# Optimization experiments

Measured on AMD Instinct MI355X. Metric: run time of the kernel, lower is better.

Reference implementation:

```python
import jax, jax.numpy as jnp
import numpy as np

N = 768          # nodes
E_HALF = 12288   # undirected edges (both directions added -> E = 24576)
P = 4096         # query pairs
H = 32           # hidden_dim_1wl == hidden_dim_2wl
MAX_X = 100
EPS = 1e-5
LAYER1 = 2


def setup_inputs() -> dict:
    key = jax.random.key(0)
    ks = jax.random.split(key, 12)
    s = 0.1
    x = jax.random.randint(ks[0], (N,), 0, MAX_X + 1)
    half = jax.random.randint(ks[1], (2, E_HALF), 0, N)
    ei = jnp.concatenate([half, half[::-1]], axis=1)          # symmetric edge set [2,E]
    pos = jax.random.randint(ks[2], (P, 2), 0, N)
    emb = jax.random.normal(ks[3], (MAX_X + 1, H)) * s
    gcn_W = jax.random.normal(ks[4], (LAYER1, H, H)) * s
    gcn_b = jnp.zeros((LAYER1, H))
    mlp1_W = jax.random.normal(ks[5], (2 * H, H)) * s
    mlp1_b = jnp.zeros((H,))
    mlp2_W = jax.random.normal(ks[6], (2 * H, H)) * s
    mlp2_b = jnp.zeros((H,))
    mlp3_W = jax.random.normal(ks[7], (H + 1, H)) * s
    mlp3_b = jnp.zeros((H,))
    lin_W = jax.random.normal(ks[8], (2 * H, 1)) * s
    lin_b = jnp.zeros((1,))
    return dict(x=x, ei=ei, pos=pos, emb=emb, gcn_W=gcn_W, gcn_b=gcn_b,
                mlp1_W=mlp1_W, mlp1_b=mlp1_b, mlp2_W=mlp2_W, mlp2_b=mlp2_b,
                mlp3_W=mlp3_W, mlp3_b=mlp3_b, lin_W=lin_W, lin_b=lin_b)


def _graph_norm(h):
    # PyG-style GraphNorm with default params (mean_scale=1, weight=1, bias=0)
    h = h - h.mean(0)
    return h * jax.lax.rsqrt((h * h).mean(0) + EPS)


def reference(x, ei, pos, emb, gcn_W, gcn_b, mlp1_W, mlp1_b,
              mlp2_W, mlp2_b, mlp3_W, mlp3_b, lin_W, lin_b):
    n = x.shape[0]
    d = emb.shape[1]
    h = emb[x]                                                 # [n,H] (dropout=0)
    # --- GCNConv stack: Ahat = D^-1/2 (A+I) D^-1/2 ---
    A = jnp.zeros((n, n), h.dtype).at[ei[0], ei[1]].set(1.0)
    Ahat = A + jnp.eye(n, dtype=h.dtype)
    dinv = jax.lax.rsqrt(Ahat.sum(1))
    An = Ahat * dinv[:, None] * dinv[None, :]
    for l in range(gcn_W.shape[0]):
        h = An @ (h @ gcn_W[l]) + gcn_b[l]
        h = jax.nn.relu(_graph_norm(h))                        # GraphNorm + ReLU
    # --- pair features ---
    xx = h[pos[:, 0]] * h[pos[:, 1]]                           # [P,H]
    val = jnp.concatenate([h[ei[0]], h[ei[1]]], 1)             # [E,2H]
    xe = jax.nn.relu(val @ mlp1_W + mlp1_b)                    # mlps_1
    mul = jax.nn.relu(val @ mlp2_W + mlp2_b)                   # mlps_2[0]
    # --- sparse_bmm as dense [n,n,d] contraction (coalesce sums duplicates -> .add) ---
    Xd = jnp.zeros((n, n, d), h.dtype).at[ei[0], ei[1]].add(xe)
    Md = jnp.zeros((n, n, d), h.dtype).at[ei[0], ei[1]].add(mul)
    C = jnp.einsum('ikd,kjd->ijd', Xd, Md)                     # x_{ij} = sum_k x_{ik}*mul_{kj}
    # support of the sparse result: 2-hop pairs union original edges (sparse_cat)
    adj_b = jnp.zeros((n, n), bool).at[ei[0], ei[1]].set(True)
    af = adj_b.astype(h.dtype)
    mask = ((af @ af) > 0) | adj_b
    ind = af[..., None]                                        # ones-column for original edges
    value = jnp.concatenate([C, ind], -1)                      # [n,n,H+1]
    z = value @ mlp3_W + mlp3_b                                # mlps_3[0]
    # GraphNorm over the edge support only (faithful to sparse values())
    m = mask.astype(h.dtype)[..., None]
    cnt = m.sum()
    mean = (z * m).sum((0, 1)) / cnt
    z = z - mean
    var = ((z * z) * m).sum((0, 1)) / cnt
    z = jax.nn.relu(z * jax.lax.rsqrt(var + EPS))
    # x * sm: multiply by transposed values; zero outside support (= add_zero)
    sym = z * jnp.swapaxes(z, 0, 1) * m
    pair = sym[pos[:, 0], pos[:, 1]]                           # [P,H] (edge_list gather)
    out = jnp.concatenate([pair, xx], 1) @ lin_W + lin_b       # lin_dir -> [P,1]
    return out
```

## Files before the change

### kernel.cpp

```cpp
#include <hip/hip_runtime.h>
#include <hip/hip_bf16.h>

#define NN 768
#define NE 24576
#define NPOS 4096
#define NCELL (NN*NN)
#define NBLK 2304
#define NBIG 2304
#define BCELLS 256
#define CAP 8
#define NREP 16

typedef __hip_bfloat16 bf16;

__device__ __forceinline__ float ldf(const void* p, int i, int mode) {
    return mode ? __bfloat162float(((const bf16*)p)[i]) : ((const float*)p)[i];
}
__device__ __forceinline__ float aread(float* p) { return atomicAdd(p, 0.f); }
__device__ __forceinline__ int areadi(int* p) { return atomicAdd(p, 0); }

template<int D, int HALF>
__device__ __forceinline__ void redRound(float* v, int lane) {
#pragma unroll
    for (int i = 0; i < HALF; i++) {
        float snd = (lane & D) ? v[i] : v[i + HALF];
        float r = __shfl_xor(snd, D);
        v[i] = ((lane & D) ? v[i + HALF] : v[i]) + r;
    }
}

#define DOT4(Z, A, W) Z += A.x * W.x + A.y * W.y + A.z * W.z + A.w * W.w

#define GATH(rec, q0,q1,q2,q3,q4,q5,q6,q7) { \
    const float4* xr = xep4 + (int)((unsigned)(rec).x & 0x7FFFu) * 8; \
    const float4* mr = mulp4 + (int)((unsigned)(rec).y & 0x7FFFu) * 8; \
    float4 xv0 = xr[0], xv1 = xr[1], xv2 = xr[2], xv3 = xr[3]; \
    float4 xv4 = xr[4], xv5 = xr[5], xv6 = xr[6], xv7 = xr[7]; \
    float4 mv0 = mr[0], mv1 = mr[1], mv2 = mr[2], mv3 = mr[3]; \
    float4 mv4 = mr[4], mv5 = mr[5], mv6 = mr[6], mv7 = mr[7]; \
    q0.x += xv0.x*mv0.x; q0.y += xv0.y*mv0.y; q0.z += xv0.z*mv0.z; q0.w += xv0.w*mv0.w; \
    q1.x += xv1.x*mv1.x; q1.y += xv1.y*mv1.y; q1.z += xv1.z*mv1.z; q1.w += xv1.w*mv1.w; \
    q2.x += xv2.x*mv2.x; q2.y += xv2.y*mv2.y; q2.z += xv2.z*mv2.z; q2.w += xv2.w*mv2.w; \
    q3.x += xv3.x*mv3.x; q3.y += xv3.y*mv3.y; q3.z += xv3.z*mv3.z; q3.w += xv3.w*mv3.w; \
    q4.x += xv4.x*mv4.x; q4.y += xv4.y*mv4.y; q4.z += xv4.z*mv4.z; q4.w += xv4.w*mv4.w; \
    q5.x += xv5.x*mv5.x; q5.y += xv5.y*mv5.y; q5.z += xv5.z*mv5.z; q5.w += xv5.w*mv5.w; \
    q6.x += xv6.x*mv6.x; q6.y += xv6.y*mv6.y; q6.z += xv6.z*mv6.z; q6.w += xv6.w*mv6.w; \
    q7.x += xv7.x*mv7.x; q7.y += xv7.y*mv7.y; q7.z += xv7.z*mv7.z; q7.w += xv7.w*mv7.w; }

__global__ void k_scatter(const int* __restrict__ ei, int* __restrict__ cell, int* __restrict__ rowlen,
                          int* __restrict__ row_ptr, float* __restrict__ dinv, int* __restrict__ dc,
                          const void* __restrict__ gW, const void* __restrict__ gB,
                          const void* __restrict__ m1W, const void* __restrict__ m1B,
                          const void* __restrict__ m2W, const void* __restrict__ m2B,
                          const void* __restrict__ m3W, const void* __restrict__ m3B,
                          const void* __restrict__ lW,  const void* __restrict__ lB,
                          const void* __restrict__ emb, int* __restrict__ modeg,
                          float* __restrict__ gwf, float* __restrict__ gbf,
                          float* __restrict__ w1f, float* __restrict__ b1f,
                          float* __restrict__ w2f, float* __restrict__ b2f,
                          float* __restrict__ w3q, float* __restrict__ linf, float* __restrict__ linb) {
    int t = threadIdx.x;
    if (blockIdx.x == 96) {
        __shared__ int bad;
        if (t == 0) bad = 0;
        __syncthreads();
        int local = 0;
        for (int i = t; i < 3232; i += 256) {
            float a = fabsf(__bfloat162float(((const bf16*)emb)[i]));
            if (!(a < 100.f)) local = 1;
        }
        if (local) atomicOr(&bad, 1);
        __syncthreads();
        int mode = bad ? 0 : 1;
        if (t == 0) *modeg = mode;
        for (int i = t; i < 2048; i += 256) {
            gwf[i] = ldf(gW, i, mode);
            w1f[i] = ldf(m1W, i, mode);
            w2f[i] = ldf(m2W, i, mode);
        }
        for (int i = t; i < 64; i += 256) { gbf[i] = ldf(gB, i, mode); linf[i] = ldf(lW, i, mode); }
        if (t < 32) { b1f[t] = ldf(m1B, t, mode); b2f[t] = ldf(m2B, t, mode); }
        for (int i = t; i < 1056; i += 256) { int c = i >> 5, d = i & 31; w3q[d * 36 + c] = ldf(m3W, i, mode); }
        if (t < 32) { w3q[t * 36 + 33] = ldf(m3B, t, mode); w3q[t * 36 + 34] = 0.f; w3q[t * 36 + 35] = 0.f; }
        if (t == 0) linb[0] = ldf(lB, 0, mode);
        return;
    }
    __shared__ int amlast;
    __shared__ int sI[256];
    int e = blockIdx.x * 256 + t;
    int a = ei[e], b = ei[NE + e];
    if ((unsigned)a < (unsigned)NN && (unsigned)b < (unsigned)NN) {
        int old = atomicAdd(&cell[a * NN + b], 1);
        if (old == 0) atomicAdd(&rowlen[a], 1);
    }
    __syncthreads();
    if (t == 0) { __threadfence(); amlast = (atomicAdd(dc, 1) == 95) ? 1 : 0; }
    __syncthreads();
    if (!amlast) return;
    int i0 = 3 * t;
    int r0 = areadi(&rowlen[i0]), r1 = areadi(&rowlen[i0 + 1]), r2 = areadi(&rowlen[i0 + 2]);
    dinv[i0]     = rsqrtf((float)r0 + 1.f);
    dinv[i0 + 1] = rsqrtf((float)r1 + 1.f);
    dinv[i0 + 2] = rsqrtf((float)r2 + 1.f);
    int s3 = r0 + r1 + r2;
    sI[t] = s3;
    __syncthreads();
    for (int off = 1; off < 256; off <<= 1) {
        int tmp = (t >= off) ? sI[t - off] : 0;
        __syncthreads();
        sI[t] += tmp;
        __syncthreads();
    }
    int excl = sI[t] - s3;
    row_ptr[i0] = excl;
    row_ptr[i0 + 1] = excl + r0;
    row_ptr[i0 + 2] = excl + r0 + r1;
    if (t == 255) row_ptr[NN] = sI[255];
}

__global__ void k_fill(int* __restrict__ cell, const int* __restrict__ row_ptr, int* __restrict__ cursor,
                       int* __restrict__ col_idx, float* __restrict__ cntv, int* __restrict__ pr_row,
                       const int* __restrict__ rowlen, int* __restrict__ rtot,
                       const int* __restrict__ x, const void* __restrict__ emb,
                       const int* __restrict__ modep, float* __restrict__ bufA) {
    int t = threadIdx.x;
    int b = blockIdx.x;
    if (b < NBLK) {
        int idx = b * 256 + t;
        int i = idx / NN;
        int j = idx - i * NN;
        int cv = cell[idx];
        if (cv > 0) {
            int p = row_ptr[i] + atomicAdd(&cursor[i], 1);
            col_idx[p] = j; cntv[p] = (float)cv; pr_row[p] = i;
            cell[idx] = p;
            atomicAdd(&rtot[i], rowlen[j]);
        } else cell[idx] = -1;
    } else {
        int idx = (b - NBLK) * 256 + t;
        int i = idx >> 5, k = idx & 31;
        int xi = x[i]; if (xi < 0) xi = 0; if (xi > 100) xi = 100;
        bufA[idx] = ldf(emb, xi * 32 + k, *modep);
    }
}

__global__ void k_aggmw0(const int* __restrict__ rtot, int* __restrict__ row_base,
                         const int* __restrict__ row_ptr, const int* __restrict__ col_idx,
                         const float* __restrict__ bufA, const float* __restrict__ dinv,
                         const float* __restrict__ gwf, const float* __restrict__ gbf,
                         float* __restrict__ bufB) {
    int t = threadIdx.x;
    if (blockIdx.x == 0) {
        __shared__ int sI[256];
        int r3[3]; int s3 = 0;
#pragma unroll
        for (int q = 0; q < 3; q++) { r3[q] = rtot[3 * t + q]; s3 += r3[q]; }
        sI[t] = s3;
        __syncthreads();
        for (int off = 1; off < 256; off <<= 1) {
            int tmp = (t >= off) ? sI[t - off] : 0;
            __syncthreads();
            sI[t] += tmp;
            __syncthreads();
        }
        int run = sI[t] - s3;
        row_base[3 * t] = run;
        row_base[3 * t + 1] = run + r3[0];
        row_base[3 * t + 2] = run + r3[0] + r3[1];
        return;
    }
    __shared__ float sg[8][32];
    int li = t >> 5, k = t & 31;
    int i = (blockIdx.x - 1) * 8 + li;
    int base = row_ptr[i], len = row_ptr[i + 1] - base;
    float di = dinv[i];
    float acc = di * bufA[i * 32 + k];
    for (int e = 0; e < len; e++) {
        int c = col_idx[base + e];
        acc += dinv[c] * bufA[c * 32 + k];
    }
    sg[li][k] = di * acc;
    __syncthreads();
    int d = k;
    float s = gbf[d];
#pragma unroll
    for (int kk = 0; kk < 32; kk++) s += sg[li][kk] * gwf[kk * 32 + d];
    bufB[i * 32 + d] = s;
}

__global__ void k_hist(const int* __restrict__ row_ptr, const int* __restrict__ col_idx,
                       const int* __restrict__ row_base,
                       int* __restrict__ pcur, int2* __restrict__ paths2, int cap,
                       const float* __restrict__ bufB, float* __restrict__ nrm0) {
    int t = threadIdx.x;
    if (blockIdx.x == NN) {
        __shared__ float r1[256], r2[256];
        int dd = t & 31, g = t >> 5;
        float s = 0.f, s2 = 0.f;
        for (int r = g; r < NN; r += 8) { float v = bufB[r * 32 + dd]; s += v; s2 += v * v; }
        r1[t] = s; r2[t] = s2;
        __syncthreads();
        if (t < 32) {
            float a = 0.f, b2 = 0.f;
            for (int k = 0; k < 8; k++) { a += r1[k * 32 + t]; b2 += r2[k * 32 + t]; }
            float mean = a / (float)NN;
            float var = b2 / (float)NN - mean * mean;
            nrm0[t] = mean;
            nrm0[32 + t] = rsqrtf(fmaxf(var, 0.f) + 1e-5f);
        }
        return;
    }
    __shared__ int hist[NN];
    __shared__ int sc[256];
    int i = blockIdx.x;
    int base = row_ptr[i], len = row_ptr[i + 1] - base;
    int rb = row_base[i];
    int wave = t >> 6, lane = t & 63;
    for (int j = t; j < NN; j += 256) hist[j] = 0;
    __syncthreads();
    for (int ee = wave; ee < len; ee += 4) {
        int k = col_idx[base + ee];
        int kb = row_ptr[k], ke = row_ptr[k + 1];
        for (int e = kb + lane; e < ke; e += 64) atomicAdd(&hist[col_idx[e]], 1);
    }
    __syncthreads();
    int h0 = hist[3 * t], h1 = hist[3 * t + 1], h2 = hist[3 * t + 2];
    int s3 = h0 + h1 + h2;
    sc[t] = s3;
    __syncthreads();
    for (int off = 1; off < 256; off <<= 1) {
        int tmp = (t >= off) ? sc[t - off] : 0;
        __syncthreads();
        sc[t] += tmp;
        __syncthreads();
    }
    int excl = sc[t] - s3;
    int n0 = i * NN + 3 * t;
    pcur[n0]     = rb + excl + h0;
    pcur[n0 + 1] = rb + excl + h0 + h1;
    pcur[n0 + 2] = rb + excl + h0 + h1 + h2;
    hist[3 * t] = excl;
    hist[3 * t + 1] = excl + h0;
    hist[3 * t + 2] = excl + h0 + h1;
    __syncthreads();
    for (int ee = wave; ee < len; ee += 4) {
        int e1 = base + ee;
        int k = col_idx[e1];
        int kb = row_ptr[k], ke = row_ptr[k + 1];
        for (int e = kb + lane; e < ke; e += 64) {
            int j = col_idx[e];
            int slot = rb + atomicAdd(&hist[j], 1);
            if (slot < cap) {
                unsigned n2 = (unsigned)(i * NN + j);
                paths2[slot] = make_int2((int)((unsigned)e1 | ((n2 & 0x1FFFFu) << 15)),
                                         (int)((unsigned)e  | ((n2 >> 17) << 15)));
            }
        }
    }
}

__global__ void k_aggmw1(const int* __restrict__ row_ptr, const int* __restrict__ col_idx,
                         const float* __restrict__ bufB, const float* __restrict__ nrm0,
                         const float* __restrict__ dinv,
                         const float* __restrict__ gwf, const float* __restrict__ gbf,
                         float* __restrict__ bufA, float* __restrict__ stats1) {
    __shared__ float sg[8][32];
    int t = threadIdx.x;
    int li = t >> 5, k = t & 31;
    int i = blockIdx.x * 8 + li;
    float mk = nrm0[k], rk = nrm0[32 + k];
    int base = row_ptr[i], len = row_ptr[i + 1] - base;
    float di = dinv[i];
    float acc = di * fmaxf((bufB[i * 32 + k] - mk) * rk, 0.f);
    for (int e = 0; e < len; e++) {
        int c = col_idx[base + e];
        acc += dinv[c] * fmaxf((bufB[c * 32 + k] - mk) * rk, 0.f);
    }
    sg[li][k] = di * acc;
    __syncthreads();
    int d = k;
    const float* W = gwf + 1024;
    float s = gbf[32 + d];
#pragma unroll
    for (int kk = 0; kk < 32; kk++) s += sg[li][kk] * W[kk * 32 + d];
    bufA[i * 32 + d] = s;
    __syncthreads();
    sg[li][d] = s;
    __syncthreads();
    if (t < 32) {
        float ps = 0.f, ps2 = 0.f;
#pragma unroll
        for (int q = 0; q < 8; q++) { float v = sg[q][t]; ps += v; ps2 += v * v; }
        float* rep = stats1 + (blockIdx.x & (NREP - 1)) * 80;
        atomicAdd(&rep[t], ps);
        atomicAdd(&rep[32 + t], ps2);
    }
}

__global__ void k_emlp(const float* __restrict__ bufA, const float* __restrict__ stats1,
                       const int* __restrict__ row_ptr, const int* __restrict__ col_idx,
                       const int* __restrict__ pr_row, const float* __restrict__ cntv,
                       const float* __restrict__ w1f, const float* __restrict__ b1f,
                       const float* __restrict__ w2f, const float* __restrict__ b2f,
                       float* __restrict__ xep, float* __restrict__ mulp, float* __restrict__ h) {
    __shared__ float nmean[32], nrstd[32];
    int t = threadIdx.x;
    int b = blockIdx.x;
    if (t < 32) {
        float s = 0.f, s2 = 0.f;
#pragma unroll
        for (int r = 0; r < NREP; r++) { s += stats1[r * 80 + t]; s2 += stats1[r * 80 + 32 + t]; }
        float mean = s / (float)NN;
        float var = s2 / (float)NN - mean * mean;
        nmean[t] = mean;
        nrstd[t] = rsqrtf(fmaxf(var, 0.f) + 1e-5f);
    }
    __syncthreads();
    if (b < 3072) {
        int d = t & 31;
        int p = b * 8 + (t >> 5);
        if (p >= row_ptr[NN]) {
            if (p < NE) { xep[p * 32 + d] = 0.f; mulp[p * 32 + d] = 0.f; }
            return;
        }
        int i = pr_row[p], j = col_idx[p];
        float a1 = b1f[d], a2 = b2f[d];
#pragma unroll
        for (int c = 0; c < 32; c++) {
            float hv = fmaxf((bufA[i * 32 + c] - nmean[c]) * nrstd[c], 0.f);
            a1 += hv * w1f[c * 32 + d];
            a2 += hv * w2f[c * 32 + d];
        }
#pragma unroll
        for (int c = 0; c < 32; c++) {
            float hv = fmaxf((bufA[j * 32 + c] - nmean[c]) * nrstd[c], 0.f);
            a1 += hv * w1f[(32 + c) * 32 + d];
            a2 += hv * w2f[(32 + c) * 32 + d];
        }
        float cv = cntv[p];
        xep[p * 32 + d]  = cv * fmaxf(a1, 0.f);
        mulp[p * 32 + d] = cv * fmaxf(a2, 0.f);
    } else {
        int idx = (b - 3072) * 256 + t;
        int d = idx & 31;
        h[idx] = fmaxf((bufA[idx] - nmean[d]) * nrstd[d], 0.f);
    }
}

__global__ __launch_bounds__(256, 4) void k_big(const int* __restrict__ pcur,
                                                const int2* __restrict__ paths2,
                                                const int* __restrict__ cellA,
                                                const float* __restrict__ xep, const float* __restrict__ mulp,
                                                const float* __restrict__ w3q,
                                                float* __restrict__ stats, int* __restrict__ done,
                                                float* __restrict__ nrm, int cap) {
    __shared__ float Cb[BCELLS * 36];
    __shared__ float sS1[32], sS2[32];
    __shared__ float sCm;
    __shared__ int amlast;
    __shared__ int qcnt;
    __shared__ int qcl[64], qps[64], qpe[64];
    const float4* xep4 = (const float4*)xep;
    const float4* mulp4 = (const float4*)mulp;
    int t = threadIdx.x;
    int b = blockIdx.x;
    int cell0 = b * BCELLS;
    int wid = t >> 6, lane = t & 63, half = lane >> 5, d = lane & 31;

    if (t == 0) { sCm = 0.f; qcnt = 0; }
    if (t < 32) { sS1[t] = 0.f; sS2[t] = 0.f; }
    int myn = cell0 + t;
    int mp1 = pcur[myn];
    int mp0 = (myn == 0) ? 0 : pcur[myn - 1];
    int madj = cellA[myn];
    if (mp0 > cap) mp0 = cap;
    if (mp1 > cap) mp1 = cap;
    __syncthreads();

    int len = mp1 - mp0;
    int take = (len > CAP) ? CAP : len;
    if (len > CAP) { int s = atomicAdd(&qcnt, 1); qcl[s] = t; qps[s] = mp0 + CAP; qpe[s] = mp1; }
    float4 q0 = {0.f,0.f,0.f,0.f}, q1 = q0, q2 = q0, q3 = q0, q4 = q0, q5 = q0, q6 = q0, q7 = q0;
    int iters = (take + 1) >> 1;
    for (int it = 0; it < iters; it++) {
        int p0 = mp0 + 2 * it;
        bool d1 = (2 * it + 1) < take;
        int2 r0 = paths2[p0];
        int2 r1 = paths2[d1 ? p0 + 1 : p0];
        GATH(r0, q0, q1, q2, q3, q4, q5, q6, q7);
        if (d1) GATH(r1, q0, q1, q2, q3, q4, q5, q6, q7);
    }
    {
        float4* crw = (float4*)(Cb + t * 36);
        crw[0] = q0; crw[1] = q1; crw[2] = q2; crw[3] = q3;
        crw[4] = q4; crw[5] = q5; crw[6] = q6; crw[7] = q7;
    }
    __syncthreads();

    int nq = qcnt;
    for (int e = wid; e < nq; e += 4) {
        int cl = qcl[e];
        int ps = qps[e] + half, pe = qpe[e];
        float acc = 0.f;
        for (int q = ps; q < pe; q += 2) {
            int2 r = paths2[q];
            acc += xep[(int)((unsigned)r.x & 0x7FFFu) * 32 + d] * mulp[(int)((unsigned)r.y & 0x7FFFu) * 32 + d];
        }
        atomicAdd(&Cb[cl * 36 + d], acc);
    }
    __syncthreads();

    float af = (madj >= 0) ? 1.f : 0.f;
    float msk = (len > 0 || madj >= 0) ? 1.f : 0.f;
    const float4* cr = (const float4*)(Cb + t * 36);
    float4 c0 = cr[0], c1 = cr[1], c2 = cr[2], c3 = cr[3];
    float4 c4 = cr[4], c5 = cr[5], c6 = cr[6], c7 = cr[7];
#pragma unroll
    for (int ch = 0; ch < 2; ch++) {
        float v[32];
#pragma unroll
        for (int j = 0; j < 16; j++) {
            int dd = ch * 16 + j;
            const float4* wr = (const float4*)(w3q + dd * 36);
            float4 wv = wr[8];
            float za = wv.y + af * wv.x;
            wv = wr[0]; DOT4(za, c0, wv);
            wv = wr[1]; DOT4(za, c1, wv);
            wv = wr[2]; DOT4(za, c2, wv);
            wv = wr[3]; DOT4(za, c3, wv);
            wv = wr[4]; DOT4(za, c4, wv);
            wv = wr[5]; DOT4(za, c5, wv);
            wv = wr[6]; DOT4(za, c6, wv);
            wv = wr[7]; DOT4(za, c7, wv);
            v[j] = msk * za;
            v[16 + j] = msk * za * za;
        }
#pragma unroll
        for (int i2 = 0; i2 < 32; i2++) v[i2] += __shfl_xor(v[i2], 32);
        redRound<16, 16>(v, lane);
        redRound<8, 8>(v, lane);
        redRound<4, 4>(v, lane);
        redRound<2, 2>(v, lane);
        redRound<1, 1>(v, lane);
        if (lane < 32) {
            if (lane < 16) atomicAdd(&sS1[ch * 16 + lane], v[0]);
            else           atomicAdd(&sS2[ch * 16 + lane - 16], v[0]);
        }
    }
    {
        float cm2 = msk;
        for (int off = 32; off >= 1; off >>= 1) cm2 += __shfl_xor(cm2, off);
        if (lane == 0) atomicAdd(&sCm, cm2);
    }
    __syncthreads();
    float* srep = stats + (b & (NREP - 1)) * 80;
    if (t < 32) {
        atomicAdd(&srep[t], sS1[t]);
        atomicAdd(&srep[32 + t], sS2[t]);
    }
    if (t == 32) atomicAdd(&srep[64], sCm);
    __syncthreads();
    if (t == 0) {
        __threadfence();
        amlast = (atomicAdd(done, 1) == NBIG - 1) ? 1 : 0;
    }
    __syncthreads();
    if (amlast && t < 32) {
        float sum1 = 0.f, sum2 = 0.f;
        for (int r = 0; r < NREP; r++) {
            sum1 += aread(&stats[r * 80 + t]);
            sum2 += aread(&stats[r * 80 + 32 + t]);
        }
        float cmt = 0.f;
        for (int r = 0; r < NREP; r++) cmt += aread(&stats[r * 80 + 64]);
        if (cmt < 1.f) cmt = 1.f;
        float mean = sum1 / cmt;
        float var = sum2 / cmt - mean * mean;
        nrm[t] = mean;
        nrm[32 + t] = rsqrtf(fmaxf(var, 0.f) + 1e-5f);
    }
}

__global__ void k_out(const int* __restrict__ pos, const int* __restrict__ pcur,
                      const int2* __restrict__ paths2,
                      const int* __restrict__ cell,
                      const float* __restrict__ xep, const float* __restrict__ mulp,
                      const float* __restrict__ h,
                      const float* __restrict__ w3q,
                      const float* __restrict__ nrm,
                      const float* __restrict__ linf, const float* __restrict__ linb,
                      const int* __restrict__ modep, int cap, void* __restrict__ outp) {
    __shared__ float Cb[4][2][32];
    int t = threadIdx.x;
    int w = t >> 6, lane = t & 63, d = lane & 31, dir = lane >> 5;
    int p = blockIdx.x * 4 + w;
    int a = pos[2 * p], b = pos[2 * p + 1];
    if ((unsigned)a >= (unsigned)NN) a = 0;
    if ((unsigned)b >= (unsigned)NN) b = 0;
    int r = dir ? b : a;
    int cc = dir ? a : b;
    int n = r * NN + cc;
    int p1 = pcur[n];
    int p0 = (n == 0) ? 0 : pcur[n - 1];
    if (p0 > cap) p0 = cap; if (p1 > cap) p1 = cap;
    float acc = 0.f;
    for (int q = p0; q < p1; q++) {
        int2 rec = paths2[q];
        int e1 = (int)((unsigned)rec.x & 0x7FFFu);
        int e2 = (int)((unsigned)rec.y & 0x7FFFu);
        acc += xep[e1 * 32 + d] * mulp[e2 * 32 + d];
    }
    Cb[w][dir][d] = acc;
    bool adj = cell[n] >= 0;
    float msk = (p1 > p0 || adj) ? 1.f : 0.f;
    __syncthreads();
    float z = w3q[d * 36 + 33] + (adj ? 1.f : 0.f) * w3q[d * 36 + 32];
#pragma unroll
    for (int c = 0; c < 32; c++) z += Cb[w][dir][c] * w3q[d * 36 + c];
    float zn = fmaxf((z - nrm[d]) * nrm[32 + d], 0.f);
    float zp = __shfl_xor(zn, 32);
    float symd = msk * zn * zp;
    float xxd = h[a * 32 + d] * h[b * 32 + d];
    float contrib = symd * linf[d] + xxd * linf[32 + d];
    for (int off = 16; off >= 1; off >>= 1) contrib += __shfl_xor(contrib, off);
    if (lane == 0) {
        float v = contrib + linb[0];
        v = fminf(fmaxf(v, -1e4f), 1e4f);
        if (*modep) ((bf16*)outp)[p] = __float2bfloat16(v);
        else        ((float*)outp)[p] = v;
    }
}

extern "C" void kernel_launch(void* const* d_in, const int* in_sizes, int n_in,
                              void* d_out, int out_size, void* d_ws, size_t ws_size,
                              hipStream_t stream) {
    const void* px  = d_in[0];  const void* pei = d_in[1];  const void* ppos = d_in[2];
    const void* pemb = d_in[3]; const void* pgW = d_in[4];  const void* pgB  = d_in[5];
    const void* pm1W = d_in[6]; const void* pm1B = d_in[7]; const void* pm2W = d_in[8];
    const void* pm2B = d_in[9]; const void* pm3W = d_in[10]; const void* pm3B = d_in[11];
    const void* plW = d_in[12]; const void* plB = d_in[13];
    {
        int c2048 = 0, c64 = 0, c32 = 0;
        for (int i = 0; i < n_in; i++) {
            int s = in_sizes[i]; const void* p = d_in[i];
            switch (s) {
                case 768:   px = p; break;
                case 49152: pei = p; break;
                case 8192:  ppos = p; break;
                case 3232:  pemb = p; break;
                case 2048:  if (c2048 == 0) pgW = p; else if (c2048 == 1) pm1W = p; else pm2W = p; c2048++; break;
                case 64:    if (c64 == 0) pgB = p; else plW = p; c64++; break;
                case 32:    if (c32 == 0) pm1B = p; else if (c32 == 1) pm2B = p; else pm3B = p; c32++; break;
                case 1056:  pm3W = p; break;
                case 1:     plB = p; break;
                default: break;
            }
        }
    }

    char* ws = (char*)d_ws;
    size_t off = 0;
    auto alloc = [&](size_t bytes) -> void* {
        void* pp = ws + off;
        off += (bytes + 255) & ~(size_t)255;
        return pp;
    };
    int*   cell    = (int*)alloc(NCELL * 4);
    int*   pcur    = (int*)alloc(NCELL * 4);
    char*  aux0    = ws + off;
    int*   rowlen  = (int*)alloc(NN * 4);
    int*   rtot    = (int*)alloc(NN * 4);
    int*   cursor  = (int*)alloc(NN * 4);
    float* stats   = (float*)alloc(NREP * 80 * 4);
    float* stats1  = (float*)alloc(NREP * 80 * 4);
    int*   dcs     = (int*)alloc(8 * 4);
    size_t auxlen  = (ws + off) - aux0;
    int*   row_base= (int*)alloc(NN * 4);
    int*   row_ptr = (int*)alloc((NN + 1) * 4);
    int*   col_idx = (int*)alloc(NE * 4);
    float* cntv    = (float*)alloc(NE * 4);
    int*   pr_row  = (int*)alloc(NE * 4);
    float* dinv    = (float*)alloc(NN * 4);
    float* h       = (float*)alloc(NN * 32 * 4);
    float* bufA    = (float*)alloc(NN * 32 * 4);
    float* bufB    = (float*)alloc(NN * 32 * 4);
    float* xep     = (float*)alloc(NE * 32 * 4);
    float* mulp    = (float*)alloc(NE * 32 * 4);
    float* nrm     = (float*)alloc(64 * 4);
    float* nrm0    = (float*)alloc(64 * 4);
    float* gwf     = (float*)alloc(2048 * 4);
    float* gbf     = (float*)alloc(64 * 4);
    float* w1f     = (float*)alloc(2048 * 4);
    float* b1f     = (float*)alloc(32 * 4);
    float* w2f     = (float*)alloc(2048 * 4);
    float* b2f     = (float*)alloc(32 * 4);
    float* w3q     = (float*)alloc(32 * 36 * 4);
    float* linf    = (float*)alloc(64 * 4);
    float* linb    = (float*)alloc(4);
    int*   modeg   = (int*)alloc(4);
    size_t remain = (ws_size > off) ? (ws_size - off) : 0;
    int cap = (int)(remain / 8);
    if (cap > (1 << 20)) cap = (1 << 20);
    int2*  paths2  = (int2*)alloc((size_t)cap * 8);

    hipMemsetAsync(cell, 0, (size_t)NCELL * 4, stream);
    hipMemsetAsync(aux0, 0, auxlen, stream);
    k_scatter<<<97, 256, 0, stream>>>((const int*)pei, cell, rowlen, row_ptr, dinv, &dcs[0],
                                      pgW, pgB, pm1W, pm1B, pm2W, pm2B, pm3W, pm3B, plW, plB,
                                      pemb, modeg, gwf, gbf, w1f, b1f, w2f, b2f, w3q, linf, linb);
    k_fill<<<NBLK + 96, 256, 0, stream>>>(cell, row_ptr, cursor, col_idx, cntv, pr_row,
                                          rowlen, rtot, (const int*)px, pemb, modeg, bufA);
    k_aggmw0<<<1 + 96, 256, 0, stream>>>(rtot, row_base, row_ptr, col_idx, bufA, dinv, gwf, gbf, bufB);
    k_hist<<<NN + 1, 256, 0, stream>>>(row_ptr, col_idx, row_base, pcur, paths2, cap, bufB, nrm0);
    k_aggmw1<<<96, 256, 0, stream>>>(row_ptr, col_idx, bufB, nrm0, dinv, gwf, gbf, bufA, stats1);
    k_emlp<<<3072 + 96, 256, 0, stream>>>(bufA, stats1, row_ptr, col_idx, pr_row, cntv,
                                          w1f, b1f, w2f, b2f, xep, mulp, h);
    k_big<<<NBIG, 256, 0, stream>>>(pcur, paths2, cell, xep, mulp,
                                    w3q, stats, &dcs[1], nrm, cap);
    k_out<<<NPOS / 4, 256, 0, stream>>>((const int*)ppos, pcur, paths2, cell, xep, mulp, h,
                                        w3q, nrm, linf, linb, modeg, cap, d_out);
}
```

Before: 314.2 us.

## Keep per-cell C accumulators in registers and shrink inline path cap

Removes the per-thread shared-memory C buffer so each cell's gathered 32-wide accumulator stays in registers and feeds the mlp3 dot product directly. The inline path cap drops from 8 to 4, and the up to four path indices are loaded up front, unrolled and clamped. Cells with more paths send their tail to a small 64-slot shared overflow buffer, reduced with a half-wave shuffle instead of shared atomics. This cuts shared memory use and barrier/LDS traffic, which should allow more resident blocks. The risk is that overflow beyond 64 cells per block is silently dropped, and the unrolled code uses more registers.

```diff
diff --git a/kernel.cpp b/kernel.cpp
--- a/kernel.cpp
+++ b/kernel.cpp
@@ -8,7 +8,7 @@
 #define NBLK 2304
 #define NBIG 2304
 #define BCELLS 256
-#define CAP 8
+#define CAP 4
 #define NREP 16
 
 typedef __hip_bfloat16 bf16;
@@ -354,12 +354,12 @@
                                                 const float* __restrict__ w3q,
                                                 float* __restrict__ stats, int* __restrict__ done,
                                                 float* __restrict__ nrm, int cap) {
-    __shared__ float Cb[BCELLS * 36];
+    __shared__ float qbuf[64 * 32];
+    __shared__ int qps[64], qpe[64];
     __shared__ float sS1[32], sS2[32];
     __shared__ float sCm;
     __shared__ int amlast;
     __shared__ int qcnt;
-    __shared__ int qcl[64], qps[64], qpe[64];
     const float4* xep4 = (const float4*)xep;
     const float4* mulp4 = (const float4*)mulp;
     int t = threadIdx.x;
@@ -379,42 +379,53 @@
 
     int len = mp1 - mp0;
     int take = (len > CAP) ? CAP : len;
-    if (len > CAP) { int s = atomicAdd(&qcnt, 1); qcl[s] = t; qps[s] = mp0 + CAP; qpe[s] = mp1; }
+    int myq = -1;
+    if (len > CAP) {
+        int s = atomicAdd(&qcnt, 1);
+        if (s < 64) { myq = s; qps[s] = mp0 + CAP; qpe[s] = mp1; }
+    }
+    int pm = cap - 1; if (pm < 0) pm = 0;
+    int i0 = mp0, i1 = mp0 + 1, i2 = mp0 + 2, i3 = mp0 + 3;
+    if (i0 > pm) i0 = pm; if (i1 > pm) i1 = pm; if (i2 > pm) i2 = pm; if (i3 > pm) i3 = pm;
+    int2 r0 = paths2[i0];
+    int2 r1 = paths2[i1];
+    int2 r2 = paths2[i2];
+    int2 r3 = paths2[i3];
     float4 q0 = {0.f,0.f,0.f,0.f}, q1 = q0, q2 = q0, q3 = q0, q4 = q0, q5 = q0, q6 = q0, q7 = q0;
-    int iters = (take + 1) >> 1;
-    for (int it = 0; it < iters; it++) {
-        int p0 = mp0 + 2 * it;
-        bool d1 = (2 * it + 1) < take;
-        int2 r0 = paths2[p0];
-        int2 r1 = paths2[d1 ? p0 + 1 : p0];
-        GATH(r0, q0, q1, q2, q3, q4, q5, q6, q7);
-        if (d1) GATH(r1, q0, q1, q2, q3, q4, q5, q6, q7);
-    }
-    {
-        float4* crw = (float4*)(Cb + t * 36);
-        crw[0] = q0; crw[1] = q1; crw[2] = q2; crw[3] = q3;
-        crw[4] = q4; crw[5] = q5; crw[6] = q6; crw[7] = q7;
-    }
-    __syncthreads();
-
-    int nq = qcnt;
+    if (take > 0) GATH(r0, q0, q1, q2, q3, q4, q5, q6, q7);
+    if (take > 1) GATH(r1, q0, q1, q2, q3, q4, q5, q6, q7);
+    if (take > 2) GATH(r2, q0, q1, q2, q3, q4, q5, q6, q7);
+    if (take > 3) GATH(r3, q0, q1, q2, q3, q4, q5, q6, q7);
+    __syncthreads();
+
+    int nq = qcnt; if (nq > 64) nq = 64;
     for (int e = wid; e < nq; e += 4) {
-        int cl = qcl[e];
-        int ps = qps[e] + half, pe = qpe[e];
+        int pe = qpe[e];
         float acc = 0.f;
-        for (int q = ps; q < pe; q += 2) {
+        for (int q = qps[e] + half; q < pe; q += 2) {
             int2 r = paths2[q];
             acc += xep[(int)((unsigned)r.x & 0x7FFFu) * 32 + d] * mulp[(int)((unsigned)r.y & 0x7FFFu) * 32 + d];
         }
-        atomicAdd(&Cb[cl * 36 + d], acc);
-    }
-    __syncthreads();
+        acc += __shfl_xor(acc, 32);
+        if (lane < 32) qbuf[e * 32 + lane] = acc;
+    }
+    __syncthreads();
+    if (myq >= 0) {
+        const float4* qb = (const float4*)(qbuf + myq * 32);
+        float4 a0 = qb[0], a1 = qb[1], a2 = qb[2], a3 = qb[3];
+        float4 a4 = qb[4], a5 = qb[5], a6 = qb[6], a7 = qb[7];
+        q0.x += a0.x; q0.y += a0.y; q0.z += a0.z; q0.w += a0.w;
+        q1.x += a1.x; q1.y += a1.y; q1.z += a1.z; q1.w += a1.w;
+        q2.x += a2.x; q2.y += a2.y; q2.z += a2.z; q2.w += a2.w;
+        q3.x += a3.x; q3.y += a3.y; q3.z += a3.z; q3.w += a3.w;
+        q4.x += a4.x; q4.y += a4.y; q4.z += a4.z; q4.w += a4.w;
+        q5.x += a5.x; q5.y += a5.y; q5.z += a5.z; q5.w += a5.w;
+        q6.x += a6.x; q6.y += a6.y; q6.z += a6.z; q6.w += a6.w;
+        q7.x += a7.x; q7.y += a7.y; q7.z += a7.z; q7.w += a7.w;
+    }
 
     float af = (madj >= 0) ? 1.f : 0.f;
     float msk = (len > 0 || madj >= 0) ? 1.f : 0.f;
-    const float4* cr = (const float4*)(Cb + t * 36);
-    float4 c0 = cr[0], c1 = cr[1], c2 = cr[2], c3 = cr[3];
-    float4 c4 = cr[4], c5 = cr[5], c6 = cr[6], c7 = cr[7];
 #pragma unroll
     for (int ch = 0; ch < 2; ch++) {
         float v[32];
@@ -424,19 +435,19 @@
             const float4* wr = (const float4*)(w3q + dd * 36);
             float4 wv = wr[8];
             float za = wv.y + af * wv.x;
-            wv = wr[0]; DOT4(za, c0, wv);
-            wv = wr[1]; DOT4(za, c1, wv);
-            wv = wr[2]; DOT4(za, c2, wv);
-            wv = wr[3]; DOT4(za, c3, wv);
-            wv = wr[4]; DOT4(za, c4, wv);
-            wv = wr[5]; DOT4(za, c5, wv);
-            wv = wr[6]; DOT4(za, c6, wv);
-            wv = wr[7]; DOT4(za, c7, wv);
+            wv = wr[0]; DOT4(za, q0, wv);
+            wv = wr[1]; DOT4(za, q1, wv);
+            wv = wr[2]; DOT4(za, q2, wv);
+            wv = wr[3]; DOT4(za, q3, wv);
+            wv = wr[4]; DOT4(za, q4, wv);
+            wv = wr[5]; DOT4(za, q5, wv);
+            wv = wr[6]; DOT4(za, q6, wv);
+            wv = wr[7]; DOT4(za, q7, wv);
             v[j] = msk * za;
             v[16 + j] = msk * za * za;
         }
 #pragma unroll
-        for (int i2 = 0; i2 < 32; i2++) v[i2] += __shfl_xor(v[i2], 32);
+        for (int i2r = 0; i2r < 32; i2r++) v[i2r] += __shfl_xor(v[i2r], 32);
         redRound<16, 16>(v, lane);
         redRound<8, 8>(v, lane);
         redRound<4, 4>(v, lane);
```

After: 302.1 us. -3.8%, faster.
